# Performance work log

Measured on AMD Instinct MI355X. Metric: run time of the kernel, lower is better.

The kernel has to match this reference:

```python
import jax, jax.numpy as jnp
import numpy as np

B, T, H = 4096, 1024, 15


def setup_inputs() -> dict:
    key = jax.random.key(0)
    ks = jax.random.split(key, 7)
    return {
        "x": jax.random.normal(ks[0], (B, T, 1), dtype=jnp.float32),
        "w_ih": jax.random.normal(ks[1], (H, 1), dtype=jnp.float32) * (1.0 / np.sqrt(H)),
        "w_hh": jax.random.normal(ks[2], (H, H), dtype=jnp.float32) * (1.0 / np.sqrt(H)),
        "b_ih": jax.random.normal(ks[3], (H,), dtype=jnp.float32) * (1.0 / np.sqrt(H)),
        "b_hh": jax.random.normal(ks[4], (H,), dtype=jnp.float32) * (1.0 / np.sqrt(H)),
        "w_lin": jax.random.normal(ks[5], (1, H), dtype=jnp.float32) * (1.0 / np.sqrt(H)),
        "b_lin": jax.random.normal(ks[6], (1,), dtype=jnp.float32) * (1.0 / np.sqrt(H)),
    }


def reference(x, w_ih, w_hh, b_ih, b_hh, w_lin, b_lin):
    # Single-layer tanh RNN (batch_first), then per-timestep linear head.
    # Precompute the input projection for all timesteps: [B, T, H]
    xp = jnp.einsum("bti,hi->bth", x, w_ih) + b_ih + b_hh
    xp_t = jnp.swapaxes(xp, 0, 1)  # [T, B, H] for scan over time

    def step(h, xt):
        # h: [B, H], xt: [B, H]
        h_new = jnp.tanh(xt + h @ w_hh.T)
        return h_new, h_new

    h0 = jnp.zeros((x.shape[0], w_hh.shape[0]), dtype=x.dtype)
    _, hs = jax.lax.scan(step, h0, xp_t)  # hs: [T, B, H]
    hs = jnp.swapaxes(hs, 0, 1)  # [B, T, H]
    return jnp.einsum("bth,oh->bto", hs, w_lin) + b_lin  # [B, T, 1]
```

## Files before the change

kernel.cpp:

```cpp
#include <hip/hip_runtime.h>

#define B_ 4096
#define T_ 1024
#define H_ 15

#define STEP(XT, ODST)                                                        \
  do {                                                                        \
    float bs_, cB_, cC_, cD_, e_;                                             \
    asm("v_fma_f32 %[bs], %[xt], %[wih], %[bias]\n\t"                         \
        "v_mul_f32_dpp %[acc], %[u], %[w1] row_ror:1 row_mask:0xf bank_mask:0xf\n\t"  \
        "v_mul_f32_dpp %[cB], %[u], %[w2] row_ror:2 row_mask:0xf bank_mask:0xf\n\t"   \
        "v_mul_f32_dpp %[cC], %[u], %[w3] row_ror:3 row_mask:0xf bank_mask:0xf\n\t"   \
        "v_fma_f32 %[cD], %[u], %[w0], %[bs]\n\t"                             \
        "v_fmac_f32_dpp %[acc], %[u], %[w5] row_ror:5 row_mask:0xf bank_mask:0xf\n\t" \
        "v_fmac_f32_dpp %[cB], %[u], %[w6] row_ror:6 row_mask:0xf bank_mask:0xf\n\t"  \
        "v_fmac_f32_dpp %[cC], %[u], %[w7] row_ror:7 row_mask:0xf bank_mask:0xf\n\t"  \
        "v_fmac_f32_dpp %[cD], %[u], %[w4] row_ror:4 row_mask:0xf bank_mask:0xf\n\t"  \
        "v_fmac_f32_dpp %[acc], %[u], %[w9] row_ror:9 row_mask:0xf bank_mask:0xf\n\t" \
        "v_fmac_f32_dpp %[cB], %[u], %[w10] row_ror:10 row_mask:0xf bank_mask:0xf\n\t" \
        "v_fmac_f32_dpp %[cC], %[u], %[w11] row_ror:11 row_mask:0xf bank_mask:0xf\n\t" \
        "v_fmac_f32_dpp %[cD], %[u], %[w8] row_ror:8 row_mask:0xf bank_mask:0xf\n\t"  \
        "v_fmac_f32_dpp %[acc], %[u], %[w13] row_ror:13 row_mask:0xf bank_mask:0xf\n\t" \
        "v_fmac_f32_dpp %[cB], %[u], %[w14] row_ror:14 row_mask:0xf bank_mask:0xf\n\t" \
        "v_fmac_f32_dpp %[cC], %[u], %[w15] row_ror:15 row_mask:0xf bank_mask:0xf\n\t" \
        "v_fmac_f32_dpp %[cD], %[u], %[w12] row_ror:12 row_mask:0xf bank_mask:0xf\n\t" \
        "v_add_f32 %[acc], %[acc], %[cB]\n\t"                                 \
        "v_add_f32 %[cC], %[cC], %[cD]\n\t"                                   \
        "v_add_f32 %[acc], %[acc], %[cC]\n\t"                                 \
        "v_exp_f32 %[e], %[acc]\n\t"                                          \
        "s_nop 0\n\t"                                                         \
        "v_add_f32 %[e], 1.0, %[e]\n\t"                                       \
        "v_rcp_f32 %[u], %[e]\n\t"                                            \
        "s_nop 0\n\t"                                                         \
        : [u] "+v"(u), [acc] "=&v"(ODST), [bs] "=&v"(bs_), [cB] "=&v"(cB_),   \
          [cC] "=&v"(cC_), [cD] "=&v"(cD_), [e] "=&v"(e_)                     \
        : [xt] "v"(XT), [wih] "v"(wih2), [bias] "v"(bias2),                   \
          [w0] "v"(wr[0]), [w1] "v"(wr[1]), [w2] "v"(wr[2]),                  \
          [w3] "v"(wr[3]), [w4] "v"(wr[4]), [w5] "v"(wr[5]),                  \
          [w6] "v"(wr[6]), [w7] "v"(wr[7]), [w8] "v"(wr[8]),                  \
          [w9] "v"(wr[9]), [w10] "v"(wr[10]), [w11] "v"(wr[11]),              \
          [w12] "v"(wr[12]), [w13] "v"(wr[13]), [w14] "v"(wr[14]),            \
          [w15] "v"(wr[15]));                                                 \
  } while (0)

#define POS(K, XV)                                                            \
  do {                                                                        \
    float o_;                                                                 \
    STEP(XV, o_);                                                             \
    osta[((K) + 3) & 3] = o_;                                                 \
    if (((K) & 3) == 0) {                                                     \
      if ((K) > 0 || t > 0) {                                                 \
        if (m == 15)                                                          \
          *(float4*)(ob + t + (K) - 4) =                                      \
              make_float4(osta[0], osta[1], osta[2], osta[3]);                \
      }                                                                       \
    }                                                                         \
    if (((K) & 3) == 3) {                                                     \
      int _tn = t + 32 + (((K) >> 2) << 2);                                   \
      if (_tn >= T_) _tn = 0;          \
      qq[(K) >> 2] = *(const float4*)(xb + _tn);                              \
    }                                                                         \
  } while (0)

__global__ __attribute__((amdgpu_flat_work_group_size(256, 256),
                          amdgpu_waves_per_eu(1, 1)))
void rnn_tanh_kernel(
    const float* __restrict__ x, const float* __restrict__ w_ih,
    const float* __restrict__ w_hh, const float* __restrict__ b_ih,
    const float* __restrict__ b_hh, const float* __restrict__ w_lin,
    const float* __restrict__ b_lin, float* __restrict__ out) {
  const int tid = threadIdx.x;
  const int m = tid & 15;
  const int b = blockIdx.x * 16 + (tid >> 4);

  const float S = 2.8853900817779268f;

  float wsum = b_lin[0];
  for (int j = 0; j < H_; ++j) wsum += w_lin[j];
  const float C = wsum;

  float wr[16];
#pragma unroll
  for (int n = 0; n < 16; ++n) {
    const int c = (m - n) & 15;
    if (m < H_)
      wr[n] = (c < H_) ? -2.0f * S * w_hh[m * H_ + c] : 0.0f;
    else
      wr[n] = (c < H_) ? -2.0f * w_lin[c] : 0.0f;
  }
  float rowsum = 0.0f;
  if (m < H_)
    for (int j = 0; j < H_; ++j) rowsum += w_hh[m * H_ + j];
  const float wih2  = (m < H_) ? S * w_ih[m] : 0.0f;
  const float bias2 = (m < H_) ? S * (b_ih[m] + b_hh[m] + rowsum) : C;

  const float* xb = x + (size_t)b * T_;
  float* ob = out + (size_t)b * T_;

  float u = 0.5f;
  asm("s_nop 1" : "+v"(u));
  float osta[4];

  float4 qq[8];
#pragma unroll
  for (int j = 0; j < 8; ++j) qq[j] = *(const float4*)(xb + 4 * j);

  for (int t = 0; t < T_; t += 32) {
    POS(0,  qq[0].x); POS(1,  qq[0].y); POS(2,  qq[0].z); POS(3,  qq[0].w);
    POS(4,  qq[1].x); POS(5,  qq[1].y); POS(6,  qq[1].z); POS(7,  qq[1].w);
    POS(8,  qq[2].x); POS(9,  qq[2].y); POS(10, qq[2].z); POS(11, qq[2].w);
    POS(12, qq[3].x); POS(13, qq[3].y); POS(14, qq[3].z); POS(15, qq[3].w);
    POS(16, qq[4].x); POS(17, qq[4].y); POS(18, qq[4].z); POS(19, qq[4].w);
    POS(20, qq[5].x); POS(21, qq[5].y); POS(22, qq[5].z); POS(23, qq[5].w);
    POS(24, qq[6].x); POS(25, qq[6].y); POS(26, qq[6].z); POS(27, qq[6].w);
    POS(28, qq[7].x); POS(29, qq[7].y); POS(30, qq[7].z); POS(31, qq[7].w);
  }

  {
    float o_;
    STEP(0.0f, o_);
    osta[3] = o_;
    if (m == 15)
      *(float4*)(ob + T_ - 4) = make_float4(osta[0], osta[1], osta[2], osta[3]);
  }
}

extern "C" void kernel_launch(void* const* d_in, const int* in_sizes, int n_in,
                              void* d_out, int out_size, void* d_ws, size_t ws_size,
                              hipStream_t stream) {
  (void)in_sizes; (void)n_in; (void)out_size; (void)d_ws; (void)ws_size;
  rnn_tanh_kernel<<<B_ / 16, 256, 0, stream>>>(
      (const float*)d_in[0], (const float*)d_in[1], (const float*)d_in[2],
      (const float*)d_in[3], (const float*)d_in[4], (const float*)d_in[5],
      (const float*)d_in[6], (float*)d_out);
}
```

Before: 140.8 us.

## Split each sequence's recurrence across two lane groups with permlane32 swap reduction

Each batch row is now handled by two 16-lane groups, one in each half of the wave, and each group computes eight of the sixteen rotated DPP products. The partial sums are combined with v_permlane32_swap plus a row_ror:8 DPP move. This shortens the per-timestep dependency chain, which is latency-bound. The input projection fma is moved off the critical path by computing it one step ahead, and occupancy rises to two waves per EU with twice the blocks. In exchange, the number of lanes per batch row doubles and the cross-lane exchange adds latency and needs nops.

```diff
diff --git a/kernel.cpp b/kernel.cpp
--- a/kernel.cpp
+++ b/kernel.cpp
@@ -4,43 +4,40 @@
 #define T_ 1024
 #define H_ 15
 
-#define STEP(XT, ODST)                                                        \
+#define STEP(XTN, ODST)                                                       \
   do {                                                                        \
-    float bs_, cB_, cC_, cD_, e_;                                             \
-    asm("v_fma_f32 %[bs], %[xt], %[wih], %[bias]\n\t"                         \
-        "v_mul_f32_dpp %[acc], %[u], %[w1] row_ror:1 row_mask:0xf bank_mask:0xf\n\t"  \
-        "v_mul_f32_dpp %[cB], %[u], %[w2] row_ror:2 row_mask:0xf bank_mask:0xf\n\t"   \
-        "v_mul_f32_dpp %[cC], %[u], %[w3] row_ror:3 row_mask:0xf bank_mask:0xf\n\t"   \
-        "v_fma_f32 %[cD], %[u], %[w0], %[bs]\n\t"                             \
-        "v_fmac_f32_dpp %[acc], %[u], %[w5] row_ror:5 row_mask:0xf bank_mask:0xf\n\t" \
-        "v_fmac_f32_dpp %[cB], %[u], %[w6] row_ror:6 row_mask:0xf bank_mask:0xf\n\t"  \
-        "v_fmac_f32_dpp %[cC], %[u], %[w7] row_ror:7 row_mask:0xf bank_mask:0xf\n\t"  \
-        "v_fmac_f32_dpp %[cD], %[u], %[w4] row_ror:4 row_mask:0xf bank_mask:0xf\n\t"  \
-        "v_fmac_f32_dpp %[acc], %[u], %[w9] row_ror:9 row_mask:0xf bank_mask:0xf\n\t" \
-        "v_fmac_f32_dpp %[cB], %[u], %[w10] row_ror:10 row_mask:0xf bank_mask:0xf\n\t" \
-        "v_fmac_f32_dpp %[cC], %[u], %[w11] row_ror:11 row_mask:0xf bank_mask:0xf\n\t" \
-        "v_fmac_f32_dpp %[cD], %[u], %[w8] row_ror:8 row_mask:0xf bank_mask:0xf\n\t"  \
-        "v_fmac_f32_dpp %[acc], %[u], %[w13] row_ror:13 row_mask:0xf bank_mask:0xf\n\t" \
-        "v_fmac_f32_dpp %[cB], %[u], %[w14] row_ror:14 row_mask:0xf bank_mask:0xf\n\t" \
-        "v_fmac_f32_dpp %[cC], %[u], %[w15] row_ror:15 row_mask:0xf bank_mask:0xf\n\t" \
-        "v_fmac_f32_dpp %[cD], %[u], %[w12] row_ror:12 row_mask:0xf bank_mask:0xf\n\t" \
-        "v_add_f32 %[acc], %[acc], %[cB]\n\t"                                 \
-        "v_add_f32 %[cC], %[cC], %[cD]\n\t"                                   \
-        "v_add_f32 %[acc], %[acc], %[cC]\n\t"                                 \
-        "v_exp_f32 %[e], %[acc]\n\t"                                          \
+    float c1_, c2_, c3_, c4_, t12_, t34_, P_, P2_, Z_, e_;                    \
+    asm("v_mul_f32_dpp %[c1], %[u], %[w1] row_ror:1 row_mask:0xf bank_mask:0xf\n\t" \
+        "v_fma_f32 %[c2], %[u], %[w0], %[bs]\n\t"                             \
+        "v_mul_f32_dpp %[c3], %[u], %[w3] row_ror:3 row_mask:0xf bank_mask:0xf\n\t" \
+        "v_mul_f32_dpp %[c4], %[u], %[w2] row_ror:2 row_mask:0xf bank_mask:0xf\n\t" \
+        "v_fmac_f32_dpp %[c1], %[u], %[w5] row_ror:5 row_mask:0xf bank_mask:0xf\n\t" \
+        "v_fmac_f32_dpp %[c2], %[u], %[w4] row_ror:4 row_mask:0xf bank_mask:0xf\n\t" \
+        "v_fmac_f32_dpp %[c3], %[u], %[w7] row_ror:7 row_mask:0xf bank_mask:0xf\n\t" \
+        "v_fmac_f32_dpp %[c4], %[u], %[w6] row_ror:6 row_mask:0xf bank_mask:0xf\n\t" \
+        "v_fma_f32 %[bs], %[xtn], %[wih], %[bias]\n\t"                        \
+        "v_add_f32 %[t12], %[c1], %[c2]\n\t"                                  \
+        "v_add_f32 %[t34], %[c3], %[c4]\n\t"                                  \
+        "v_add_f32 %[P], %[t12], %[t34]\n\t"                                  \
+        "v_add_f32 %[P2], %[t12], %[t34]\n\t"                                 \
+        "s_nop 1\n\t"                                                         \
+        "v_permlane32_swap_b32 %[P], %[P2]\n\t"                               \
+        "s_nop 1\n\t"                                                         \
+        "v_mov_b32_dpp %[Z], %[P2] row_ror:8 row_mask:0xf bank_mask:0xf\n\t"  \
+        "v_add_f32 %[aF], %[P], %[Z]\n\t"                                     \
+        "v_exp_f32 %[e], %[aF]\n\t"                                           \
         "s_nop 0\n\t"                                                         \
         "v_add_f32 %[e], 1.0, %[e]\n\t"                                       \
         "v_rcp_f32 %[u], %[e]\n\t"                                            \
-        "s_nop 0\n\t"                                                         \
-        : [u] "+v"(u), [acc] "=&v"(ODST), [bs] "=&v"(bs_), [cB] "=&v"(cB_),   \
-          [cC] "=&v"(cC_), [cD] "=&v"(cD_), [e] "=&v"(e_)                     \
-        : [xt] "v"(XT), [wih] "v"(wih2), [bias] "v"(bias2),                   \
-          [w0] "v"(wr[0]), [w1] "v"(wr[1]), [w2] "v"(wr[2]),                  \
-          [w3] "v"(wr[3]), [w4] "v"(wr[4]), [w5] "v"(wr[5]),                  \
-          [w6] "v"(wr[6]), [w7] "v"(wr[7]), [w8] "v"(wr[8]),                  \
-          [w9] "v"(wr[9]), [w10] "v"(wr[10]), [w11] "v"(wr[11]),              \
-          [w12] "v"(wr[12]), [w13] "v"(wr[13]), [w14] "v"(wr[14]),            \
-          [w15] "v"(wr[15]));                                                 \
+        "s_nop 1\n\t"                                                         \
+        : [u] "+v"(u), [bs] "+v"(bs), [aF] "=&v"(ODST),                       \
+          [c1] "=&v"(c1_), [c2] "=&v"(c2_), [c3] "=&v"(c3_), [c4] "=&v"(c4_), \
+          [t12] "=&v"(t12_), [t34] "=&v"(t34_), [P] "=&v"(P_),                \
+          [P2] "=&v"(P2_), [Z] "=&v"(Z_), [e] "=&v"(e_)                       \
+        : [xtn] "v"(XTN), [wih] "v"(wih2), [bias] "v"(bias2),                 \
+          [w0] "v"(wr2[0]), [w1] "v"(wr2[1]), [w2] "v"(wr2[2]),               \
+          [w3] "v"(wr2[3]), [w4] "v"(wr2[4]), [w5] "v"(wr2[5]),               \
+          [w6] "v"(wr2[6]), [w7] "v"(wr2[7]));                                \
   } while (0)
 
 #define POS(K, XV)                                                            \
@@ -50,7 +47,7 @@
     osta[((K) + 3) & 3] = o_;                                                 \
     if (((K) & 3) == 0) {                                                     \
       if ((K) > 0 || t > 0) {                                                 \
-        if (m == 15)                                                          \
+        if ((tid & 47) == 15)                                                 \
           *(float4*)(ob + t + (K) - 4) =                                      \
               make_float4(osta[0], osta[1], osta[2], osta[3]);                \
       }                                                                       \
@@ -63,7 +60,7 @@
   } while (0)
 
 __global__ __attribute__((amdgpu_flat_work_group_size(256, 256),
-                          amdgpu_waves_per_eu(1, 1)))
+                          amdgpu_waves_per_eu(2, 2)))
 void rnn_tanh_kernel(
     const float* __restrict__ x, const float* __restrict__ w_ih,
     const float* __restrict__ w_hh, const float* __restrict__ b_ih,
@@ -71,7 +68,10 @@
     const float* __restrict__ b_lin, float* __restrict__ out) {
   const int tid = threadIdx.x;
   const int m = tid & 15;
-  const int b = blockIdx.x * 16 + (tid >> 4);
+  const int r = (tid >> 4) & 3;
+  const int half = r >> 1;
+  const int q = r & 1;
+  const int b = blockIdx.x * 8 + ((tid >> 6) << 1) + q;
 
   const float S = 2.8853900817779268f;
 
@@ -79,20 +79,24 @@
   for (int j = 0; j < H_; ++j) wsum += w_lin[j];
   const float C = wsum;
 
-  float wr[16];
+  const int p = half ? ((m + 8) & 15) : m;
+  float wr2[8];
 #pragma unroll
-  for (int n = 0; n < 16; ++n) {
+  for (int n = 0; n < 8; ++n) {
     const int c = (m - n) & 15;
-    if (m < H_)
-      wr[n] = (c < H_) ? -2.0f * S * w_hh[m * H_ + c] : 0.0f;
-    else
-      wr[n] = (c < H_) ? -2.0f * w_lin[c] : 0.0f;
+    float w = 0.0f;
+    if (c < H_) {
+      if (p < H_) w = -2.0f * S * w_hh[p * H_ + c];
+      else        w = -2.0f * w_lin[c];
+    }
+    wr2[n] = w;
   }
   float rowsum = 0.0f;
   if (m < H_)
     for (int j = 0; j < H_; ++j) rowsum += w_hh[m * H_ + j];
-  const float wih2  = (m < H_) ? S * w_ih[m] : 0.0f;
-  const float bias2 = (m < H_) ? S * (b_ih[m] + b_hh[m] + rowsum) : C;
+  const float wih2 = (half == 0 && m < H_) ? S * w_ih[m] : 0.0f;
+  const float bias2 =
+      (half == 0) ? ((m < H_) ? S * (b_ih[m] + b_hh[m] + rowsum) : C) : 0.0f;
 
   const float* xb = x + (size_t)b * T_;
   float* ob = out + (size_t)b * T_;
@@ -105,22 +109,24 @@
 #pragma unroll
   for (int j = 0; j < 8; ++j) qq[j] = *(const float4*)(xb + 4 * j);
 
+  float bs = fmaf(qq[0].x, wih2, bias2);
+
   for (int t = 0; t < T_; t += 32) {
-    POS(0,  qq[0].x); POS(1,  qq[0].y); POS(2,  qq[0].z); POS(3,  qq[0].w);
-    POS(4,  qq[1].x); POS(5,  qq[1].y); POS(6,  qq[1].z); POS(7,  qq[1].w);
-    POS(8,  qq[2].x); POS(9,  qq[2].y); POS(10, qq[2].z); POS(11, qq[2].w);
-    POS(12, qq[3].x); POS(13, qq[3].y); POS(14, qq[3].z); POS(15, qq[3].w);
-    POS(16, qq[4].x); POS(17, qq[4].y); POS(18, qq[4].z); POS(19, qq[4].w);
-    POS(20, qq[5].x); POS(21, qq[5].y); POS(22, qq[5].z); POS(23, qq[5].w);
-    POS(24, qq[6].x); POS(25, qq[6].y); POS(26, qq[6].z); POS(27, qq[6].w);
-    POS(28, qq[7].x); POS(29, qq[7].y); POS(30, qq[7].z); POS(31, qq[7].w);
+    POS(0,  qq[0].y); POS(1,  qq[0].z); POS(2,  qq[0].w); POS(3,  qq[1].x);
+    POS(4,  qq[1].y); POS(5,  qq[1].z); POS(6,  qq[1].w); POS(7,  qq[2].x);
+    POS(8,  qq[2].y); POS(9,  qq[2].z); POS(10, qq[2].w); POS(11, qq[3].x);
+    POS(12, qq[3].y); POS(13, qq[3].z); POS(14, qq[3].w); POS(15, qq[4].x);
+    POS(16, qq[4].y); POS(17, qq[4].z); POS(18, qq[4].w); POS(19, qq[5].x);
+    POS(20, qq[5].y); POS(21, qq[5].z); POS(22, qq[5].w); POS(23, qq[6].x);
+    POS(24, qq[6].y); POS(25, qq[6].z); POS(26, qq[6].w); POS(27, qq[7].x);
+    POS(28, qq[7].y); POS(29, qq[7].z); POS(30, qq[7].w); POS(31, qq[0].x);
   }
 
   {
     float o_;
     STEP(0.0f, o_);
     osta[3] = o_;
-    if (m == 15)
+    if ((tid & 47) == 15)
       *(float4*)(ob + T_ - 4) = make_float4(osta[0], osta[1], osta[2], osta[3]);
   }
 }
@@ -129,7 +135,7 @@
                               void* d_out, int out_size, void* d_ws, size_t ws_size,
                               hipStream_t stream) {
   (void)in_sizes; (void)n_in; (void)out_size; (void)d_ws; (void)ws_size;
-  rnn_tanh_kernel<<<B_ / 16, 256, 0, stream>>>(
+  rnn_tanh_kernel<<<B_ / 8, 256, 0, stream>>>(
       (const float*)d_in[0], (const float*)d_in[1], (const float*)d_in[2],
       (const float*)d_in[3], (const float*)d_in[4], (const float*)d_in[5],
       (const float*)d_in[6], (float*)d_out);
```

Measured after the change: 168.3 us. +19.5%, slower.
